# Optimization experiments

Measured on AMD Instinct MI355X. Metric: run time of the kernel, lower is better.

The kernel has to match this reference:

```python
import jax, jax.numpy as jnp
import numpy as np

B, F0, D = 2048, 39, 16
CROSS = [200, 200, 200]


def setup_inputs() -> dict:
    key = jax.random.key(0)
    ks = jax.random.split(key, 7)
    inp = {"x": jax.random.normal(ks[0], (B, F0, D), dtype=jnp.float32)}
    prev = F0
    for i, c in enumerate(CROSS):
        # Conv1d(in=F0*prev, out=c, kernel=1) weight reshaped to (c, F0, prev)
        scale = 1.0 / np.sqrt(F0 * prev)
        inp[f"W{i}"] = jax.random.normal(ks[1 + 2 * i], (c, F0, prev), dtype=jnp.float32) * scale
        inp[f"b{i}"] = jnp.zeros((c,), dtype=jnp.float32)
        prev = c
    return inp


def reference(x, W0, b0, W1, b1, W2, b2):
    # x: (B, F0, D). Each CIN layer in torch materializes x0*h -> (B, F0*prev, D)
    # then applies a kernel-1 Conv1d. Mathematically this is the bilinear
    # contraction below (same values, no quadratic intermediate).
    x0 = x
    h = x
    xs = []
    for W, b in ((W0, b0), (W1, b1), (W2, b2)):
        # z[b,o,d] = sum_{f,g} W[o,f,g] * x0[b,f,d] * h[b,g,d] + bias[o]
        z = jnp.einsum('bfd,bgd,ofg->bod', x0, h, W) + b[None, :, None]
        h = jax.nn.relu(z)
        xs.append(h)
    # concat over channel dim, sum-pool over embed dim -> (B, sum(cross_sizes))
    return jnp.sum(jnp.concatenate(xs, axis=1), axis=2)
```

## Files before the change

### kernel.cpp

```cpp
#include <hip/hip_runtime.h>
#include <hip/hip_bf16.h>
#include <stdint.h>

typedef __attribute__((ext_vector_type(8))) short bf16x8;
typedef __attribute__((ext_vector_type(4))) float f32x4;
typedef unsigned short u16;
typedef unsigned int u32;

__device__ __forceinline__ u16 f2bf_rne(float v) {
    u32 u = __float_as_uint(v);
    u32 r = (u + 0x7fffu + ((u >> 16) & 1u)) >> 16;
    return (u16)r;
}


__global__ void pack_x_kernel(const float* __restrict__ x, u16* __restrict__ xbd) {
    int idx = blockIdx.x * 256 + threadIdx.x;
    if (idx >= 32768 * 40) return;
    int m = idx / 40, f = idx - m * 40;
    int b = m >> 4, d = m & 15;
    float v = (f < 39) ? x[(b * 39 + f) * 16 + d] : 0.0f;
    xbd[idx] = f2bf_rne(v);
}

__global__ void pack_w0_kernel(const float* __restrict__ W, u16* __restrict__ Wp) {
    int idx = blockIdx.x * 256 + threadIdx.x;
    if (idx >= 224 * 1600) return;
    int o = idx / 1600, k = idx - o * 1600;
    int f = k / 40, g = k - f * 40;
    float v = (o < 200 && f < 39 && g < 39) ? W[(o * 39 + f) * 39 + g] : 0.0f;
    Wp[idx] = f2bf_rne(v);
}

__global__ void pack_w12_kernel(const float* __restrict__ W, u16* __restrict__ Wp) {
    int idx = blockIdx.x * 256 + threadIdx.x;
    if (idx >= 224 * 8128) return;
    int o = idx / 8128, k = idx - o * 8128;
    int f = k / 208, g = k - f * 208;
    float v = (o < 200 && f < 39 && g < 200) ? W[o * 7800 + f * 200 + g] : 0.0f;
    Wp[idx] = f2bf_rne(v);
}

template <int LAYER>
__global__ __launch_bounds__(512, 2) void cin_gemm2(
    const u16* __restrict__ Xbd,
    const u16* __restrict__ Hin,
    const u16* __restrict__ Wp,
    const float* __restrict__ bias,
    u16* __restrict__ Hout,
    float* __restrict__ out)
{
    constexpr int KP    = (LAYER == 0) ? 1600 : 8128;
    constexpr int NPAIR = KP / 64;
    constexpr int HSTR  = (LAYER == 0) ? 40 : 216;
    constexpr u32 MAGIC = (LAYER == 0) ? 3277u : 10083u;
    constexpr int SHIFT = (LAYER == 0) ? 17 : 21;
    constexpr int GCL   = (LAYER == 0) ? 32 : 200;
    constexpr int GS    = (LAYER == 0) ? 40 : 208;
    constexpr int XOFF  = (LAYER == 0) ? 0 : 110592;
    constexpr int WOFF  = XOFF + 20480;
    constexpr int SMEM  = (LAYER == 0) ? 114688 : 148992;

    __shared__ __align__(16) char smem[SMEM];
    u16* Hl = (u16*)smem;
    u16* Xl = (u16*)(smem + XOFF);
    u16* Wl = (u16*)(smem + WOFF);

    const int bid  = blockIdx.x;
    const int mblk = bid >> 1, nblk = bid & 1;
    const int m0    = mblk * 256;
    const int ncol0 = nblk * 112;
    const int NT    = nblk ? 6 : 7;
    const int tid  = threadIdx.x;
    const int lane = tid & 63, wid = tid >> 6;
    const int mg = wid & 3, kg = wid >> 2;
    const int rowl = lane & 15, grp = lane >> 4;

    for (int u = tid; u < 256 * 5; u += 512) {
        int r = u / 5, q = u - r * 5;
        *(int4*)&Xl[r * 40 + q * 8] = *(const int4*)&Xbd[(size_t)(m0 + r) * 40 + q * 8];
    }
    if constexpr (LAYER > 0) {
        for (int u = tid; u < 256 * 26; u += 512) {
            int r = u / 26, q = u - r * 26;
            *(int4*)&Hl[r * HSTR + q * 8] = *(const int4*)&Hin[(size_t)(m0 + r) * 208 + q * 8];
        }
    }
    for (int u = tid; u < 896; u += 512) {
        int c = (u >= 448) ? 1 : 0;
        int uu = u - c * 448;
        int r = uu >> 2, q = uu & 3;
        *(int4*)&Wl[c * 4480 + r * 40 + q * 8] =
            *(const int4*)&Wp[(size_t)(ncol0 + r) * KP + c * 32 + q * 8];
    }
    __syncthreads();

    int xro[4], hro[4];
    #pragma unroll
    for (int s = 0; s < 4; ++s) {
        int r = mg * 64 + s * 16 + rowl;
        xro[s] = r * 40;
        hro[s] = r * HSTR;
    }
    const u16* Hb = (LAYER == 0) ? Xl : Hl;

    f32x4 acc[4][7];
    #pragma unroll
    for (int s = 0; s < 4; ++s)
        #pragma unroll
        for (int t = 0; t < 7; ++t) {
            f32x4 z = {0.f, 0.f, 0.f, 0.f};
            acc[s][t] = z;
        }

    const int pc0 = (tid >= 448) ? 1 : 0;
    const int pu0 = tid - pc0 * 448;
    const int pr0 = pu0 >> 2, pq0 = pu0 & 3;
    const int pr1 = (tid + 64) >> 2, pq1 = (tid + 64) & 3;

    int4 pre0, pre1;
    for (int pr = 0; pr < NPAIR; ++pr) {
        const bool pf = (pr + 1 < NPAIR);
        if (pf) {
            int kb = (pr + 1) * 64;
            pre0 = *(const int4*)&Wp[(size_t)(ncol0 + pr0) * KP + kb + pc0 * 32 + pq0 * 8];
            if (tid < 384)
                pre1 = *(const int4*)&Wp[(size_t)(ncol0 + pr1) * KP + kb + 32 + pq1 * 8];
        }
        int k0 = pr * 64 + kg * 32 + grp * 8;
        u32 f = ((u32)k0 * MAGIC) >> SHIFT;
        f = (f > 38u) ? 38u : f;
        int g0 = k0 - (int)f * GS;
        g0 = (g0 > GCL) ? GCL : g0;
        bf16x8 afrag[4];
        #pragma unroll
        for (int s = 0; s < 4; ++s) {
            u16 xs = Xl[xro[s] + (int)f];
            bf16x8 hv = *(const bf16x8*)&Hb[hro[s] + g0];
            float xf = __uint_as_float(((u32)xs) << 16);
            union { bf16x8 v; u32 w[4]; } hu, au;
            hu.v = hv;
            #pragma unroll
            for (int j = 0; j < 4; ++j) {
                float lo = __uint_as_float(hu.w[j] << 16);
                float hi = __uint_as_float(hu.w[j] & 0xffff0000u);
                float pl = xf * lo;
                float ph = xf * hi;
                u32 pk;
                asm("v_cvt_pk_bf16_f32 %0, %1, %2" : "=v"(pk) : "v"(pl), "v"(ph));
                au.w[j] = pk;
            }
            afrag[s] = au.v;
        }
        const u16* wb = &Wl[kg * 4480 + rowl * 40 + grp * 8];
        #pragma unroll
        for (int t = 0; t < 7; ++t) {
            if (t < NT) {
                bf16x8 bfrag = *(const bf16x8*)&wb[t * 640];
                #pragma unroll
                for (int s = 0; s < 4; ++s)
                    acc[s][t] = __builtin_amdgcn_mfma_f32_16x16x32_bf16(afrag[s], bfrag, acc[s][t], 0, 0, 0);
            }
        }
        __syncthreads();
        if (pf) {
            *(int4*)&Wl[pc0 * 4480 + pr0 * 40 + pq0 * 8] = pre0;
            if (tid < 384)
                *(int4*)&Wl[4480 + pr1 * 40 + pq1 * 8] = pre1;
        }
        __syncthreads();
    }

    __syncthreads();
    float* red = (float*)smem;
    const int rbase = mg * 7168 + lane * 4;
    if (kg == 1) {
        #pragma unroll
        for (int s = 0; s < 4; ++s)
            #pragma unroll
            for (int t = 0; t < 7; ++t)
                if (t < NT)
                    *(f32x4*)&red[rbase + (s * 7 + t) * 256] = acc[s][t];
    }
    __syncthreads();

    if (kg == 0) {
        float bias_t[7];
        #pragma unroll
        for (int t = 0; t < 7; ++t) {
            int oc = ncol0 + t * 16 + rowl;
            bias_t[t] = (t < NT && oc < 200) ? bias[oc] : 0.0f;
        }
        #pragma unroll
        for (int s = 0; s < 4; ++s) {
            int mrow0 = m0 + mg * 64 + s * 16;
            int bidx = mrow0 >> 4;
            #pragma unroll
            for (int t = 0; t < 7; ++t) {
                if (t < NT) {
                    int oc = ncol0 + t * 16 + rowl;
                    f32x4 o = *(const f32x4*)&red[rbase + (s * 7 + t) * 256];
                    f32x4 v = acc[s][t];
                    float h0 = fmaxf(v[0] + o[0] + bias_t[t], 0.0f);
                    float h1 = fmaxf(v[1] + o[1] + bias_t[t], 0.0f);
                    float h2 = fmaxf(v[2] + o[2] + bias_t[t], 0.0f);
                    float h3 = fmaxf(v[3] + o[3] + bias_t[t], 0.0f);
                    if constexpr (LAYER < 2) {
                        size_t rb = (size_t)(mrow0 + grp * 4) * 208 + oc;
                        Hout[rb]           = f2bf_rne(h0);
                        Hout[rb + 208]     = f2bf_rne(h1);
                        Hout[rb + 2*208]   = f2bf_rne(h2);
                        Hout[rb + 3*208]   = f2bf_rne(h3);
                    }
                    float ssum = (h0 + h1) + (h2 + h3);
                    ssum += __shfl_xor(ssum, 16);
                    ssum += __shfl_xor(ssum, 32);
                    if (grp == 0 && oc < 200)
                        out[(size_t)bidx * 600 + LAYER * 200 + oc] = ssum;
                }
            }
        }
    }
}

extern "C" void kernel_launch(void* const* d_in, const int* in_sizes, int n_in,
                              void* d_out, int out_size, void* d_ws, size_t ws_size,
                              hipStream_t stream) {
    const float* x  = (const float*)d_in[0];
    const float* W0 = (const float*)d_in[1];
    const float* b0 = (const float*)d_in[2];
    const float* W1 = (const float*)d_in[3];
    const float* b1 = (const float*)d_in[4];
    const float* W2 = (const float*)d_in[5];
    const float* b2 = (const float*)d_in[6];
    float* out = (float*)d_out;

    char* ws = (char*)d_ws;
    u16* xbd = (u16*)(ws);
    u16* wp0 = (u16*)(ws + 2621440);
    u16* wp1 = (u16*)(ws + 3338240);
    u16* wp2 = (u16*)(ws + 6979584);
    u16* h1  = (u16*)(ws + 10620928);
    u16* h2  = (u16*)(ws + 24252416);

    pack_x_kernel<<<5120, 256, 0, stream>>>(x, xbd);
    pack_w0_kernel<<<1400, 256, 0, stream>>>(W0, wp0);
    pack_w12_kernel<<<7112, 256, 0, stream>>>(W1, wp1);
    pack_w12_kernel<<<7112, 256, 0, stream>>>(W2, wp2);

    cin_gemm2<0><<<256, 512, 0, stream>>>(xbd, (const u16*)nullptr, wp0, b0, h1, out);
    cin_gemm2<1><<<256, 512, 0, stream>>>(xbd, h1, wp1, b1, h2, out);
    cin_gemm2<2><<<256, 512, 0, stream>>>(xbd, h2, wp2, b2, (u16*)nullptr, out);
}
```

Baseline: 315.3 us.

## Stream weight tiles into double-buffered LDS via global_load_lds

Replaces the register-staged weight prefetch with direct global-to-LDS loads (global_load_lds) into a double-buffered weight tile, dropping one of the two barriers per K step. The X and H tiles are also loaded straight into LDS this way, using an unpadded row stride. The goal is to cut register pressure and the VGPR-to-LDS store traffic and barriers in the main loop. The risks are LDS bank conflicts from removing the row padding, and a possible ordering problem, since no explicit wait on the async loads is visible before the first reads.

```diff
diff --git a/kernel.cpp b/kernel.cpp
--- a/kernel.cpp
+++ b/kernel.cpp
@@ -6,6 +6,10 @@
 typedef __attribute__((ext_vector_type(4))) float f32x4;
 typedef unsigned short u16;
 typedef unsigned int u32;
+
+#define GLL(gp, lp) __builtin_amdgcn_global_load_lds( \
+    (const __attribute__((address_space(1))) void*)(gp), \
+    (__attribute__((address_space(3))) void*)(lp), 16, 0, 0)
 
 __device__ __forceinline__ u16 f2bf_rne(float v) {
     u32 u = __float_as_uint(v);
@@ -42,7 +46,7 @@
 }
 
 template <int LAYER>
-__global__ __launch_bounds__(512, 2) void cin_gemm2(
+__global__ __launch_bounds__(512, 2) void cin_gemm3(
     const u16* __restrict__ Xbd,
     const u16* __restrict__ Hin,
     const u16* __restrict__ Wp,
@@ -52,19 +56,18 @@
 {
     constexpr int KP    = (LAYER == 0) ? 1600 : 8128;
     constexpr int NPAIR = KP / 64;
-    constexpr int HSTR  = (LAYER == 0) ? 40 : 216;
     constexpr u32 MAGIC = (LAYER == 0) ? 3277u : 10083u;
     constexpr int SHIFT = (LAYER == 0) ? 17 : 21;
-    constexpr int GCL   = (LAYER == 0) ? 32 : 200;
     constexpr int GS    = (LAYER == 0) ? 40 : 208;
-    constexpr int XOFF  = (LAYER == 0) ? 0 : 110592;
-    constexpr int WOFF  = XOFF + 20480;
-    constexpr int SMEM  = (LAYER == 0) ? 114688 : 148992;
+    constexpr int HROW  = (LAYER == 0) ? 40 : 208;
+    constexpr int HSZ   = (LAYER == 0) ? 0 : 106496;
+    constexpr int WOFF  = 20480 + HSZ;
+    constexpr int SMEMA = WOFF + 28672;
+    constexpr int SMEM  = (SMEMA > 117760) ? SMEMA : 117760;
 
     __shared__ __align__(16) char smem[SMEM];
-    u16* Hl = (u16*)smem;
-    u16* Xl = (u16*)(smem + XOFF);
-    u16* Wl = (u16*)(smem + WOFF);
+    u16* Xl = (u16*)smem;
+    u16* Hl = (u16*)(smem + 20480);
 
     const int bid  = blockIdx.x;
     const int mblk = bid >> 1, nblk = bid & 1;
@@ -76,31 +79,40 @@
     const int mg = wid & 3, kg = wid >> 2;
     const int rowl = lane & 15, grp = lane >> 4;
 
-    for (int u = tid; u < 256 * 5; u += 512) {
-        int r = u / 5, q = u - r * 5;
-        *(int4*)&Xl[r * 40 + q * 8] = *(const int4*)&Xbd[(size_t)(m0 + r) * 40 + q * 8];
-    }
-    if constexpr (LAYER > 0) {
-        for (int u = tid; u < 256 * 26; u += 512) {
-            int r = u / 26, q = u - r * 26;
-            *(int4*)&Hl[r * HSTR + q * 8] = *(const int4*)&Hin[(size_t)(m0 + r) * 208 + q * 8];
-        }
-    }
-    for (int u = tid; u < 896; u += 512) {
+    int goff0, goff1;
+    {
+        int u = wid * 64 + lane;
         int c = (u >= 448) ? 1 : 0;
         int uu = u - c * 448;
-        int r = uu >> 2, q = uu & 3;
-        *(int4*)&Wl[c * 4480 + r * 40 + q * 8] =
-            *(const int4*)&Wp[(size_t)(ncol0 + r) * KP + c * 32 + q * 8];
-    }
-    __syncthreads();
+        goff0 = (ncol0 + (uu >> 2)) * KP + c * 32 + (uu & 3) * 8;
+        int u1 = (wid + 8) * 64 + lane;
+        int uu1 = u1 - 448;
+        goff1 = (ncol0 + (uu1 >> 2)) * KP + 32 + (uu1 & 3) * 8;
+    }
+
+    {
+        const char* xsrc = (const char*)(Xbd + (size_t)m0 * 40);
+        for (int i = wid; i < 20; i += 8)
+            GLL(xsrc + i * 1024 + lane * 16, smem + i * 1024);
+    }
+    if constexpr (LAYER > 0) {
+        const char* hsrc = (const char*)(Hin + (size_t)m0 * 208);
+        for (int i = wid; i < 104; i += 8)
+            GLL(hsrc + i * 1024 + lane * 16, smem + 20480 + i * 1024);
+    }
+    {
+        const u16* gsrc = Wp;
+        char* wb = smem + WOFF;
+        GLL((const char*)(gsrc + goff0), wb + wid * 1024);
+        if (wid < 6) GLL((const char*)(gsrc + goff1), wb + wid * 1024 + 8192);
+    }
 
     int xro[4], hro[4];
     #pragma unroll
     for (int s = 0; s < 4; ++s) {
         int r = mg * 64 + s * 16 + rowl;
         xro[s] = r * 40;
-        hro[s] = r * HSTR;
+        hro[s] = r * HROW;
     }
     const u16* Hb = (LAYER == 0) ? Xl : Hl;
 
@@ -113,25 +125,17 @@
             acc[s][t] = z;
         }
 
-    const int pc0 = (tid >= 448) ? 1 : 0;
-    const int pu0 = tid - pc0 * 448;
-    const int pr0 = pu0 >> 2, pq0 = pu0 & 3;
-    const int pr1 = (tid + 64) >> 2, pq1 = (tid + 64) & 3;
-
-    int4 pre0, pre1;
     for (int pr = 0; pr < NPAIR; ++pr) {
-        const bool pf = (pr + 1 < NPAIR);
-        if (pf) {
-            int kb = (pr + 1) * 64;
-            pre0 = *(const int4*)&Wp[(size_t)(ncol0 + pr0) * KP + kb + pc0 * 32 + pq0 * 8];
-            if (tid < 384)
-                pre1 = *(const int4*)&Wp[(size_t)(ncol0 + pr1) * KP + kb + 32 + pq1 * 8];
+        __syncthreads();
+        if (pr + 1 < NPAIR) {
+            const u16* gsrc = Wp + (size_t)(pr + 1) * 64;
+            char* wb = smem + WOFF + ((pr + 1) & 1) * 14336;
+            GLL((const char*)(gsrc + goff0), wb + wid * 1024);
+            if (wid < 6) GLL((const char*)(gsrc + goff1), wb + wid * 1024 + 8192);
         }
         int k0 = pr * 64 + kg * 32 + grp * 8;
         u32 f = ((u32)k0 * MAGIC) >> SHIFT;
-        f = (f > 38u) ? 38u : f;
         int g0 = k0 - (int)f * GS;
-        g0 = (g0 > GCL) ? GCL : g0;
         bf16x8 afrag[4];
         #pragma unroll
         for (int s = 0; s < 4; ++s) {
@@ -152,23 +156,16 @@
             }
             afrag[s] = au.v;
         }
-        const u16* wb = &Wl[kg * 4480 + rowl * 40 + grp * 8];
+        const u16* wbR = (const u16*)(smem + WOFF + (pr & 1) * 14336) + kg * 3584 + rowl * 32 + grp * 8;
         #pragma unroll
         for (int t = 0; t < 7; ++t) {
             if (t < NT) {
-                bf16x8 bfrag = *(const bf16x8*)&wb[t * 640];
+                bf16x8 bfrag = *(const bf16x8*)&wbR[t * 512];
                 #pragma unroll
                 for (int s = 0; s < 4; ++s)
                     acc[s][t] = __builtin_amdgcn_mfma_f32_16x16x32_bf16(afrag[s], bfrag, acc[s][t], 0, 0, 0);
             }
         }
-        __syncthreads();
-        if (pf) {
-            *(int4*)&Wl[pc0 * 4480 + pr0 * 40 + pq0 * 8] = pre0;
-            if (tid < 384)
-                *(int4*)&Wl[4480 + pr1 * 40 + pq1 * 8] = pre1;
-        }
-        __syncthreads();
     }
 
     __syncthreads();
@@ -248,7 +245,7 @@
     pack_w12_kernel<<<7112, 256, 0, stream>>>(W1, wp1);
     pack_w12_kernel<<<7112, 256, 0, stream>>>(W2, wp2);
 
-    cin_gemm2<0><<<256, 512, 0, stream>>>(xbd, (const u16*)nullptr, wp0, b0, h1, out);
-    cin_gemm2<1><<<256, 512, 0, stream>>>(xbd, h1, wp1, b1, h2, out);
-    cin_gemm2<2><<<256, 512, 0, stream>>>(xbd, h2, wp2, b2, (u16*)nullptr, out);
-}
+    cin_gemm3<0><<<256, 512, 0, stream>>>(xbd, (const u16*)nullptr, wp0, b0, h1, out);
+    cin_gemm3<1><<<256, 512, 0, stream>>>(xbd, h1, wp1, b1, h2, out);
+    cin_gemm3<2><<<256, 512, 0, stream>>>(xbd, h2, wp2, b2, (u16*)nullptr, out);
+}
```

New measurement: 292.4 us. 1.08x faster.
